# Kernel optimization log

Hardware: AMD Instinct MI355X
Metric: run time of the kernel (lower is better)

The kernel has to match this reference:

```python
import jax, jax.numpy as jnp
import numpy as np

EPS = 1e-10
NCE_T = 0.1
JSD_T = 1.0

def setup_inputs() -> dict:
    key = jax.random.key(0)
    k1, k2, k3, k4, k5 = jax.random.split(key, 5)
    N, D, C = 8192, 128, 1000
    return {
        'fs': jax.random.normal(k1, (N, D), dtype=jnp.float32),
        'ft': jax.random.normal(k2, (N, D), dtype=jnp.float32),
        'logit_s': jax.random.normal(k3, (N, C), dtype=jnp.float32),
        'logit_t': jax.random.normal(k4, (N, C), dtype=jnp.float32),
        'target': jax.random.randint(k5, (N,), 0, 100, dtype=jnp.int64),
    }

def _l2_normalize(x, axis=1, eps=1e-12):
    n = jnp.sqrt(jnp.sum(x * x, axis=axis, keepdims=True))
    return x / jnp.maximum(n, eps)

def _nce_loss(f1, f2, targets):
    f1 = _l2_normalize(f1)
    f2 = _l2_normalize(f2)
    # pos_mask[i,j] = 1 where targets[i] == targets[j] (same class, incl. diagonal)
    pos_mask = (targets[:, None] == targets[None, :]).astype(jnp.float32)  # [N,N]
    neg_mask = 1.0 - pos_mask
    # dist = ||f1_i - f2_j||^2 = 2 - 2 <f1_i, f2_j> for unit vectors -> cos = 1 - 0.5*dist = f1 @ f2.T
    cos = jnp.matmul(f1, f2.T)  # [N,N]
    ps = jax.nn.softmax(cos / NCE_T, axis=1)
    log_pos = -jnp.log(ps + EPS) * pos_mask
    log_neg = -jnp.log(1.0 - ps + EPS) * neg_mask
    row = log_pos.sum(1) / pos_mask.sum(1) + log_neg.sum(1) / neg_mask.sum(1)
    return row.mean()

def _jsd_loss(y_s, y_t):
    N = y_s.shape[0]
    log_ps = jax.nn.log_softmax(y_s / JSD_T, axis=1)
    log_pt = jax.nn.log_softmax(y_t / JSD_T, axis=1)
    pt = jnp.exp(log_pt)
    ps = jnp.exp(log_ps)
    # F.kl_div(input=log_p, target=q, reduction='sum') = sum(q * (log q - log_p))
    kl_st = jnp.sum(pt * (log_pt - log_ps)) * (JSD_T ** 2) / N
    kl_ts = jnp.sum(ps * (log_ps - log_pt)) * (JSD_T ** 2) / N
    return 0.5 * (kl_st + kl_ts)

def reference(fs, ft, logit_s, logit_t, target):
    return _nce_loss(fs, ft, target) + _jsd_loss(logit_s, logit_t)
```

## Files before the change

kernel.cpp:

```cpp
#include <hip/hip_runtime.h>
#include <hip/hip_bf16.h>

#define NN 8192
#define DD 128
#define CC 1000
#define LN2 0.69314718f
#define G_SCALE 14.42695041f
#define NSTRIP 16
#define JPER   512
#define NTILE  8
#define LROW   128
#define GRID_NCE 1024
#define JSD_BLOCKS 2048
#define PREP_GRID (JSD_BLOCKS + 1024 + 8)

typedef short v8s __attribute__((ext_vector_type(8)));
typedef float v4f __attribute__((ext_vector_type(4)));
typedef unsigned short u16;
typedef unsigned int u32;

typedef __attribute__((address_space(1))) const unsigned char ga_t;
typedef __attribute__((address_space(3))) unsigned char la_t;
#define GLOAD_LDS16(g, l) __builtin_amdgcn_global_load_lds((ga_t*)(g), (la_t*)(l), 16, 0, 0)

#if __has_builtin(__builtin_amdgcn_exp2f)
#define EXP2(x) __builtin_amdgcn_exp2f(x)
#else
#define EXP2(x) exp2f(x)
#endif
#if __has_builtin(__builtin_amdgcn_logf)
#define LOG2(x) __builtin_amdgcn_logf(x)
#else
#define LOG2(x) log2f(x)
#endif

static __device__ __forceinline__ float bf2f(u16 u) {
    union { float f; u32 i; } x; x.i = ((u32)u) << 16; return x.f;
}
static __device__ __forceinline__ u16 f2bf(float f) {
    u32 x = __float_as_uint(f);
    return (u16)((x + 0x7FFFu + ((x >> 16) & 1u)) >> 16);
}
static __device__ __forceinline__ float wsum(float v) {
    #pragma unroll
    for (int m = 1; m < 64; m <<= 1) v += __shfl_xor(v, m, 64);
    return v;
}
static __device__ __forceinline__ float wmax(float v) {
    #pragma unroll
    for (int m = 1; m < 64; m <<= 1) v = fmaxf(v, __shfl_xor(v, m, 64));
    return v;
}

__global__ __launch_bounds__(256) void prep_kernel(const void* __restrict__ fs,
                                                   const void* __restrict__ ft,
                                                   const int* __restrict__ traw,
                                                   const void* __restrict__ ls,
                                                   const void* __restrict__ lt,
                                                   u16* __restrict__ f1, u16* __restrict__ f2,
                                                   int* __restrict__ tgt32,
                                                   int* __restrict__ ghist,
                                                   float* __restrict__ sums) {
    __shared__ float sred[4];
    __shared__ int h[128];
    int b = blockIdx.x, tid = threadIdx.x;
    int w = tid >> 6, lane = tid & 63;

    if (b < JSD_BLOCKS) {
        int row = b * 4 + w;
        u32 wb = ((const u32*)ls)[(size_t)row * 500 + lane];
        unsigned e = (wb >> 7) & 0xFF;
        int isF32 = (__popcll(__ballot(e >= 100 && e <= 140)) < 32);

        float xs[16], xt[16];
        #pragma unroll
        for (int c = 0; c < 4; c++) {
            int idx = c * 256 + lane * 4;
            if (idx < CC) {
                if (isF32) {
                    float4 a = *(const float4*)((const float*)ls + (size_t)row * CC + idx);
                    float4 bb = *(const float4*)((const float*)lt + (size_t)row * CC + idx);
                    xs[c*4+0] = a.x; xs[c*4+1] = a.y; xs[c*4+2] = a.z; xs[c*4+3] = a.w;
                    xt[c*4+0] = bb.x; xt[c*4+1] = bb.y; xt[c*4+2] = bb.z; xt[c*4+3] = bb.w;
                } else {
                    ushort4 a = *(const ushort4*)((const u16*)ls + (size_t)row * CC + idx);
                    ushort4 bb = *(const ushort4*)((const u16*)lt + (size_t)row * CC + idx);
                    xs[c*4+0] = bf2f(a.x); xs[c*4+1] = bf2f(a.y); xs[c*4+2] = bf2f(a.z); xs[c*4+3] = bf2f(a.w);
                    xt[c*4+0] = bf2f(bb.x); xt[c*4+1] = bf2f(bb.y); xt[c*4+2] = bf2f(bb.z); xt[c*4+3] = bf2f(bb.w);
                }
            } else {
                #pragma unroll
                for (int q = 0; q < 4; q++) { xs[c*4+q] = -1e30f; xt[c*4+q] = -1e30f; }
            }
        }
        float ms = -1e30f, mt = -1e30f;
        #pragma unroll
        for (int q = 0; q < 16; q++) { ms = fmaxf(ms, xs[q]); mt = fmaxf(mt, xt[q]); }
        ms = wmax(ms); mt = wmax(mt);
        float es = 0.f, et = 0.f;
        #pragma unroll
        for (int q = 0; q < 16; q++) { es += __expf(xs[q] - ms); et += __expf(xt[q] - mt); }
        es = wsum(es); et = wsum(et);
        float lse_s = ms + __logf(es), lse_t = mt + __logf(et);
        float contrib = 0.f;
        #pragma unroll
        for (int q = 0; q < 16; q++) {
            float lps = xs[q] - lse_s, lpt = xt[q] - lse_t;
            contrib += (lpt - lps) * (__expf(lpt) - __expf(lps));
        }
        contrib = wsum(contrib);
        if (lane == 0) sred[w] = contrib;
        __syncthreads();
        if (tid == 0) atomicAdd(&sums[1], sred[0] + sred[1] + sred[2] + sred[3]);
    } else if (b < JSD_BLOCKS + 1024) {
        int nb = b - JSD_BLOCKS;
        #pragma unroll
        for (int r = 0; r < 4; r++) {
            int row4 = nb * 16 + w * 4 + r;
            const void* src; u16* dst; float gain; int row;
            if (row4 < NN) { src = fs; dst = f1; gain = G_SCALE; row = row4; }
            else           { src = ft; dst = f2; gain = 1.0f;    row = row4 - NN; }
            u32 wb = ((const u32*)src)[(size_t)row * 64 + lane];
            unsigned e = (wb >> 7) & 0xFF;
            int isF32 = (__popcll(__ballot(e >= 100 && e <= 140)) < 32);
            float x0, x1;
            if (isF32) {
                float2 v = ((const float2*)src)[(size_t)row * 64 + lane];
                x0 = v.x; x1 = v.y;
            } else {
                x0 = bf2f((u16)(wb & 0xFFFF));
                x1 = bf2f((u16)(wb >> 16));
            }
            float ss = wsum(x0 * x0 + x1 * x1);
            float sc = gain / fmaxf(sqrtf(ss), 1e-12f);
            u32 outw = (u32)f2bf(x0 * sc) | ((u32)f2bf(x1 * sc) << 16);
            ((u32*)dst)[(size_t)row * 64 + lane] = outw;
        }
    } else {
        int db = b - JSD_BLOCKS - 1024;
        if (tid < 128) h[tid] = 0;
        __syncthreads();
        #pragma unroll
        for (int r = 0; r < 4; r++) {
            int idx = db * 1024 + r * 256 + tid;
            int k = (idx >> 1) & 4095;
            int odd = traw[2 * k + 1];
            int is32 = (__ballot(odd != 0) != 0ull);
            int t = (is32 ? traw[idx] : traw[2 * idx]) & 127;
            tgt32[idx] = t;
            atomicAdd(&h[t], 1);
        }
        __syncthreads();
        if (tid < 128 && h[tid]) atomicAdd(&ghist[tid], h[tid]);
    }
}

__global__ __launch_bounds__(256) void main_kernel(const u16* __restrict__ f1,
                                                   const u16* __restrict__ f2,
                                                   const int* __restrict__ tgt,
                                                   float* __restrict__ Pp,
                                                   float* __restrict__ Qp,
                                                   float* __restrict__ Sp) {
    __shared__ u16 lds[2][64 * LROW];
    int bx = blockIdx.x;
    int tid = threadIdx.x;
    int w = tid >> 6, lane = tid & 63;

    int strip = bx & (NSTRIP - 1);
    int ib = bx >> 4;
    int quad = lane >> 4, lcol = lane & 15;
    int ibase = ib * 128 + w * 32;

    v8s a0[4], a1[4];
    #pragma unroll
    for (int t = 0; t < 4; t++) {
        int k = t * 32 + quad * 8;
        a0[t] = *(const v8s*)(f1 + (size_t)(ibase + lcol) * DD + k);
        a1[t] = *(const v8s*)(f1 + (size_t)(ibase + 16 + lcol) * DD + k);
    }
    int ti[8];
    #pragma unroll
    for (int a = 0; a < 2; a++)
        #pragma unroll
        for (int v = 0; v < 4; v++)
            ti[a * 4 + v] = tgt[ibase + a * 16 + quad * 4 + v];

    float P[8] = {}, Q[8] = {}, S[8] = {};

    int rrl = 4 * w + (lane >> 4);
    int cg = (lane & 15) ^ rrl;
    const u16* gb = f2 + (size_t)strip * JPER * DD + (size_t)rrl * DD + cg * 8;
    int ldsbase = 4 * w * 256;

    #pragma unroll
    for (int r = 0; r < 4; r++)
        GLOAD_LDS16(gb + (size_t)r * 16 * DD,
                    (unsigned char*)lds[0] + ldsbase + r * 16 * 256);

    for (int it = 0; it < NTILE; ++it) {
        __syncthreads();
        if (it + 1 < NTILE) {
            const u16* g2 = gb + (size_t)(it + 1) * 64 * DD;
            unsigned char* l2 = (unsigned char*)lds[(it + 1) & 1] + ldsbase;
            #pragma unroll
            for (int r = 0; r < 4; r++)
                GLOAD_LDS16(g2 + (size_t)r * 16 * DD, l2 + r * 16 * 256);
        }
        int jb = strip * JPER + it * 64;
        int tj0 = tgt[jb + lcol];
        int tj1 = tgt[jb + 16 + lcol];
        int tj2 = tgt[jb + 32 + lcol];
        int tj3 = tgt[jb + 48 + lcol];

        const u16* buf = lds[it & 1];
        v4f zero = {0.f, 0.f, 0.f, 0.f};
        v4f acc[8] = {zero, zero, zero, zero, zero, zero, zero, zero};
        #pragma unroll
        for (int t = 0; t < 4; t++) {
            int s = ((quad + 4 * t) ^ lcol) * 8;
            v8s b0 = *(const v8s*)(buf + (lcol)*LROW + s);
            v8s b1 = *(const v8s*)(buf + (16 + lcol) * LROW + s);
            v8s b2 = *(const v8s*)(buf + (32 + lcol) * LROW + s);
            v8s b3 = *(const v8s*)(buf + (48 + lcol) * LROW + s);
            acc[0] = __builtin_amdgcn_mfma_f32_16x16x32_bf16(a0[t], b0, acc[0], 0, 0, 0);
            acc[1] = __builtin_amdgcn_mfma_f32_16x16x32_bf16(a0[t], b1, acc[1], 0, 0, 0);
            acc[2] = __builtin_amdgcn_mfma_f32_16x16x32_bf16(a0[t], b2, acc[2], 0, 0, 0);
            acc[3] = __builtin_amdgcn_mfma_f32_16x16x32_bf16(a0[t], b3, acc[3], 0, 0, 0);
            acc[4] = __builtin_amdgcn_mfma_f32_16x16x32_bf16(a1[t], b0, acc[4], 0, 0, 0);
            acc[5] = __builtin_amdgcn_mfma_f32_16x16x32_bf16(a1[t], b1, acc[5], 0, 0, 0);
            acc[6] = __builtin_amdgcn_mfma_f32_16x16x32_bf16(a1[t], b2, acc[6], 0, 0, 0);
            acc[7] = __builtin_amdgcn_mfma_f32_16x16x32_bf16(a1[t], b3, acc[7], 0, 0, 0);
        }
        #pragma unroll
        for (int a = 0; a < 2; a++) {
            #pragma unroll
            for (int v = 0; v < 4; v++) {
                int t_i = ti[a * 4 + v];
                #pragma unroll
                for (int jf = 0; jf < 4; jf++) {
                    float s2 = acc[a * 4 + jf][v];
                    float e1 = EXP2(s2);
                    int tj = (jf == 0) ? tj0 : (jf == 1) ? tj1 : (jf == 2) ? tj2 : tj3;
                    bool pos = (tj == t_i);
                    P[a * 4 + v] += e1;
                    Q[a * 4 + v] += pos ? e1 : 0.0f;
                    S[a * 4 + v] += pos ? s2 : 0.0f;
                }
            }
        }
    }

    #pragma unroll
    for (int a = 0; a < 2; a++) {
        #pragma unroll
        for (int v = 0; v < 4; v++) {
            float p = P[a * 4 + v], q = Q[a * 4 + v], s = S[a * 4 + v];
            #pragma unroll
            for (int m = 1; m < 16; m <<= 1) {
                p += __shfl_xor(p, m, 64);
                q += __shfl_xor(q, m, 64);
                s += __shfl_xor(s, m, 64);
            }
            if (lcol == 0) {
                size_t idx = (size_t)strip * NN + ibase + a * 16 + quad * 4 + v;
                Pp[idx] = p;
                Qp[idx] = q;
                Sp[idx] = s;
            }
        }
    }
}

__global__ __launch_bounds__(256) void rowred_kernel(const float* __restrict__ Pp,
                                                     const float* __restrict__ Qp,
                                                     const float* __restrict__ Sp,
                                                     const int* __restrict__ tgt,
                                                     const int* __restrict__ ghist,
                                                     float* __restrict__ sums,
                                                     u32* __restrict__ out) {
    __shared__ float sb[4];
    __shared__ int lastf;
    int tid = threadIdx.x;

    int i = blockIdx.x * 256 + tid;
    float P = 0.f, Q = 0.f, S = 0.f;
    #pragma unroll
    for (int s = 0; s < NSTRIP; s++) {
        P += Pp[(size_t)s * NN + i];
        Q += Qp[(size_t)s * NN + i];
        S += Sp[(size_t)s * NN + i];
    }
    int cnt = ghist[tgt[i]];
    float pos = LN2 * LOG2(P) - LN2 * S / (float)cnt;
    float neg = (1.0f - Q / P) / (float)(NN - cnt);
    float l = wsum(pos + neg);
    if ((tid & 63) == 0) sb[tid >> 6] = l;
    __syncthreads();
    if (tid == 0) {
        atomicAdd(&sums[0], sb[0] + sb[1] + sb[2] + sb[3]);
        __threadfence();
        int* done = (int*)sums + 2;
        lastf = (atomicAdd(done, 1) == 31);
    }
    __syncthreads();
    if (!lastf) return;
    if (tid == 0) {
        float Lsum = __hip_atomic_load(&sums[0], __ATOMIC_RELAXED, __HIP_MEMORY_SCOPE_AGENT);
        float Jsum = __hip_atomic_load(&sums[1], __ATOMIC_RELAXED, __HIP_MEMORY_SCOPE_AGENT);
        float loss = (Lsum + 0.5f * Jsum) / (float)NN;
        u32 fb = __float_as_uint(loss);
        out[0] = (fb & 0xFFFF0000u) | (u32)f2bf(loss);
    }
}

extern "C" void kernel_launch(void* const* d_in, const int* in_sizes, int n_in,
                              void* d_out, int out_size, void* d_ws, size_t ws_size,
                              hipStream_t stream) {
    const void* fs = d_in[0];
    const void* ft = d_in[1];
    const void* ls = d_in[2];
    const void* lt = d_in[3];
    const int* tgt_raw = (const int*)d_in[4];

    char* wsp = (char*)d_ws;
    u16*   f1    = (u16*)(wsp + 0);
    u16*   f2    = (u16*)(wsp + 2097152);
    float* Pp    = (float*)(wsp + 4194304);
    float* Qp    = (float*)(wsp + 4718592);
    float* Sp    = (float*)(wsp + 5242880);
    float* sums  = (float*)(wsp + 5767168);
    int*   ghist = (int*)(wsp + 5767296);
    int*   tgt32 = (int*)(wsp + 5768192);

    hipMemsetAsync(wsp + 5767168, 0, 640, stream);
    prep_kernel<<<PREP_GRID, 256, 0, stream>>>(fs, ft, tgt_raw, ls, lt,
                                               f1, f2, tgt32, ghist, sums);
    main_kernel<<<GRID_NCE, 256, 0, stream>>>(f1, f2, tgt32, Pp, Qp, Sp);
    rowred_kernel<<<32, 256, 0, stream>>>(Pp, Qp, Sp, tgt32, ghist, sums, (u32*)d_out);
}
```

Measured before the change: 165.9 us.

## Move JSD work into the final reduction kernel and drop the memset

```diff
diff --git a/kernel.cpp b/kernel.cpp
--- a/kernel.cpp
+++ b/kernel.cpp
@@ -12,7 +12,9 @@
 #define LROW   128
 #define GRID_NCE 1024
 #define JSD_BLOCKS 2048
-#define PREP_GRID (JSD_BLOCKS + 1024 + 8)
+#define RED_BLOCKS 32
+#define GRID_JR (JSD_BLOCKS + RED_BLOCKS)
+#define DONE_TARGET GRID_JR
 
 typedef short v8s __attribute__((ext_vector_type(8)));
 typedef float v4f __attribute__((ext_vector_type(4)));
@@ -51,23 +53,198 @@
     for (int m = 1; m < 64; m <<= 1) v = fmaxf(v, __shfl_xor(v, m, 64));
     return v;
 }
+static __device__ __forceinline__ void finalize(float* sums, u32* out) {
+    float Lsum = __hip_atomic_load(&sums[0], __ATOMIC_RELAXED, __HIP_MEMORY_SCOPE_AGENT);
+    float Jsum = __hip_atomic_load(&sums[1], __ATOMIC_RELAXED, __HIP_MEMORY_SCOPE_AGENT);
+    float loss = (Lsum + 0.5f * Jsum) / (float)NN;
+    u32 fb = __float_as_uint(loss);
+    out[0] = (fb & 0xFFFF0000u) | (u32)f2bf(loss);
+}
 
 __global__ __launch_bounds__(256) void prep_kernel(const void* __restrict__ fs,
                                                    const void* __restrict__ ft,
                                                    const int* __restrict__ traw,
-                                                   const void* __restrict__ ls,
-                                                   const void* __restrict__ lt,
                                                    u16* __restrict__ f1, u16* __restrict__ f2,
                                                    int* __restrict__ tgt32,
                                                    int* __restrict__ ghist,
                                                    float* __restrict__ sums) {
-    __shared__ float sred[4];
     __shared__ int h[128];
     int b = blockIdx.x, tid = threadIdx.x;
     int w = tid >> 6, lane = tid & 63;
 
-    if (b < JSD_BLOCKS) {
-        int row = b * 4 + w;
+    if (b < 1024) {
+        #pragma unroll
+        for (int r = 0; r < 4; r++) {
+            int row4 = b * 16 + w * 4 + r;
+            const void* src; u16* dst; float gain; int row;
+            if (row4 < NN) { src = fs; dst = f1; gain = G_SCALE; row = row4; }
+            else           { src = ft; dst = f2; gain = 1.0f;    row = row4 - NN; }
+            u32 wb = ((const u32*)src)[(size_t)row * 64 + lane];
+            unsigned e = (wb >> 7) & 0xFF;
+            int isF32 = (__popcll(__ballot(e >= 100 && e <= 140)) < 32);
+            float x0, x1;
+            if (isF32) {
+                float2 v = ((const float2*)src)[(size_t)row * 64 + lane];
+                x0 = v.x; x1 = v.y;
+            } else {
+                x0 = bf2f((u16)(wb & 0xFFFF));
+                x1 = bf2f((u16)(wb >> 16));
+            }
+            float ss = wsum(x0 * x0 + x1 * x1);
+            float sc = gain / fmaxf(sqrtf(ss), 1e-12f);
+            u32 outw = (u32)f2bf(x0 * sc) | ((u32)f2bf(x1 * sc) << 16);
+            ((u32*)dst)[(size_t)row * 64 + lane] = outw;
+        }
+    } else {
+        if (tid < 4) sums[tid] = 0.0f;
+        if (tid < 128) h[tid] = 0;
+        __syncthreads();
+        for (int r = 0; r < 32; r++) {
+            int idx = r * 256 + tid;
+            int k = (idx >> 1) & 4095;
+            int odd = traw[2 * k + 1];
+            int is32 = (__ballot(odd != 0) != 0ull);
+            int t = (is32 ? traw[idx] : traw[2 * idx]) & 127;
+            tgt32[idx] = t;
+            atomicAdd(&h[t], 1);
+        }
+        __syncthreads();
+        if (tid < 128) ghist[tid] = h[tid];
+    }
+}
+
+__global__ __launch_bounds__(256) void main_kernel(const u16* __restrict__ f1,
+                                                   const u16* __restrict__ f2,
+                                                   const int* __restrict__ tgt,
+                                                   float* __restrict__ Pp,
+                                                   float* __restrict__ Qp,
+                                                   float* __restrict__ Sp) {
+    __shared__ u16 lds[2][64 * LROW];
+    int bx = blockIdx.x;
+    int tid = threadIdx.x;
+    int w = tid >> 6, lane = tid & 63;
+
+    int strip = bx & (NSTRIP - 1);
+    int ib = bx >> 4;
+    int quad = lane >> 4, lcol = lane & 15;
+    int ibase = ib * 128 + w * 32;
+
+    v8s a0[4], a1[4];
+    #pragma unroll
+    for (int t = 0; t < 4; t++) {
+        int k = t * 32 + quad * 8;
+        a0[t] = *(const v8s*)(f1 + (size_t)(ibase + lcol) * DD + k);
+        a1[t] = *(const v8s*)(f1 + (size_t)(ibase + 16 + lcol) * DD + k);
+    }
+    int ti[8];
+    #pragma unroll
+    for (int a = 0; a < 2; a++)
+        #pragma unroll
+        for (int v = 0; v < 4; v++)
+            ti[a * 4 + v] = tgt[ibase + a * 16 + quad * 4 + v];
+
+    float P[8] = {}, Q[8] = {}, S[8] = {};
+
+    int rrl = 4 * w + (lane >> 4);
+    int cg = (lane & 15) ^ rrl;
+    const u16* gb = f2 + (size_t)strip * JPER * DD + (size_t)rrl * DD + cg * 8;
+    int ldsbase = 4 * w * 256;
+
+    #pragma unroll
+    for (int r = 0; r < 4; r++)
+        GLOAD_LDS16(gb + (size_t)r * 16 * DD,
+                    (unsigned char*)lds[0] + ldsbase + r * 16 * 256);
+
+    for (int it = 0; it < NTILE; ++it) {
+        __syncthreads();
+        if (it + 1 < NTILE) {
+            const u16* g2 = gb + (size_t)(it + 1) * 64 * DD;
+            unsigned char* l2 = (unsigned char*)lds[(it + 1) & 1] + ldsbase;
+            #pragma unroll
+            for (int r = 0; r < 4; r++)
+                GLOAD_LDS16(g2 + (size_t)r * 16 * DD, l2 + r * 16 * 256);
+        }
+        int jb = strip * JPER + it * 64;
+        int tj0 = tgt[jb + lcol];
+        int tj1 = tgt[jb + 16 + lcol];
+        int tj2 = tgt[jb + 32 + lcol];
+        int tj3 = tgt[jb + 48 + lcol];
+
+        const u16* buf = lds[it & 1];
+        v4f zero = {0.f, 0.f, 0.f, 0.f};
+        v4f acc[8] = {zero, zero, zero, zero, zero, zero, zero, zero};
+        #pragma unroll
+        for (int t = 0; t < 4; t++) {
+            int s = ((quad + 4 * t) ^ lcol) * 8;
+            v8s b0 = *(const v8s*)(buf + (lcol)*LROW + s);
+            v8s b1 = *(const v8s*)(buf + (16 + lcol) * LROW + s);
+            v8s b2 = *(const v8s*)(buf + (32 + lcol) * LROW + s);
+            v8s b3 = *(const v8s*)(buf + (48 + lcol) * LROW + s);
+            acc[0] = __builtin_amdgcn_mfma_f32_16x16x32_bf16(a0[t], b0, acc[0], 0, 0, 0);
+            acc[1] = __builtin_amdgcn_mfma_f32_16x16x32_bf16(a0[t], b1, acc[1], 0, 0, 0);
+            acc[2] = __builtin_amdgcn_mfma_f32_16x16x32_bf16(a0[t], b2, acc[2], 0, 0, 0);
+            acc[3] = __builtin_amdgcn_mfma_f32_16x16x32_bf16(a0[t], b3, acc[3], 0, 0, 0);
+            acc[4] = __builtin_amdgcn_mfma_f32_16x16x32_bf16(a1[t], b0, acc[4], 0, 0, 0);
+            acc[5] = __builtin_amdgcn_mfma_f32_16x16x32_bf16(a1[t], b1, acc[5], 0, 0, 0);
+            acc[6] = __builtin_amdgcn_mfma_f32_16x16x32_bf16(a1[t], b2, acc[6], 0, 0, 0);
+            acc[7] = __builtin_amdgcn_mfma_f32_16x16x32_bf16(a1[t], b3, acc[7], 0, 0, 0);
+        }
+        #pragma unroll
+        for (int a = 0; a < 2; a++) {
+            #pragma unroll
+            for (int v = 0; v < 4; v++) {
+                int t_i = ti[a * 4 + v];
+                #pragma unroll
+                for (int jf = 0; jf < 4; jf++) {
+                    float s2 = acc[a * 4 + jf][v];
+                    float e1 = EXP2(s2);
+                    int tj = (jf == 0) ? tj0 : (jf == 1) ? tj1 : (jf == 2) ? tj2 : tj3;
+                    bool pos = (tj == t_i);
+                    P[a * 4 + v] += e1;
+                    Q[a * 4 + v] += pos ? e1 : 0.0f;
+                    S[a * 4 + v] += pos ? s2 : 0.0f;
+                }
+            }
+        }
+    }
+
+    #pragma unroll
+    for (int a = 0; a < 2; a++) {
+        #pragma unroll
+        for (int v = 0; v < 4; v++) {
+            float p = P[a * 4 + v], q = Q[a * 4 + v], s = S[a * 4 + v];
+            #pragma unroll
+            for (int m = 1; m < 16; m <<= 1) {
+                p += __shfl_xor(p, m, 64);
+                q += __shfl_xor(q, m, 64);
+                s += __shfl_xor(s, m, 64);
+            }
+            if (lcol == 0) {
+                size_t idx = (size_t)strip * NN + ibase + a * 16 + quad * 4 + v;
+                Pp[idx] = p;
+                Qp[idx] = q;
+                Sp[idx] = s;
+            }
+        }
+    }
+}
+
+__global__ __launch_bounds__(256) void jsdred_kernel(const void* __restrict__ ls,
+                                                     const void* __restrict__ lt,
+                                                     const float* __restrict__ Pp,
+                                                     const float* __restrict__ Qp,
+                                                     const float* __restrict__ Sp,
+                                                     const int* __restrict__ tgt,
+                                                     const int* __restrict__ ghist,
+                                                     float* __restrict__ sums,
+                                                     u32* __restrict__ out) {
+    __shared__ float sred[4];
+    int bx = blockIdx.x;
+    int tid = threadIdx.x;
+    int w = tid >> 6, lane = tid & 63;
+
+    if (bx < JSD_BLOCKS) {
+        int row = bx * 4 + w;
         u32 wb = ((const u32*)ls)[(size_t)row * 500 + lane];
         unsigned e = (wb >> 7) & 0xFF;
         int isF32 = (__popcll(__ballot(e >= 100 && e <= 140)) < 32);
@@ -111,205 +288,31 @@
         contrib = wsum(contrib);
         if (lane == 0) sred[w] = contrib;
         __syncthreads();
-        if (tid == 0) atomicAdd(&sums[1], sred[0] + sred[1] + sred[2] + sred[3]);
-    } else if (b < JSD_BLOCKS + 1024) {
-        int nb = b - JSD_BLOCKS;
-        #pragma unroll
-        for (int r = 0; r < 4; r++) {
-            int row4 = nb * 16 + w * 4 + r;
-            const void* src; u16* dst; float gain; int row;
-            if (row4 < NN) { src = fs; dst = f1; gain = G_SCALE; row = row4; }
-            else           { src = ft; dst = f2; gain = 1.0f;    row = row4 - NN; }
-            u32 wb = ((const u32*)src)[(size_t)row * 64 + lane];
-            unsigned e = (wb >> 7) & 0xFF;
-            int isF32 = (__popcll(__ballot(e >= 100 && e <= 140)) < 32);
-            float x0, x1;
-            if (isF32) {
-                float2 v = ((const float2*)src)[(size_t)row * 64 + lane];
-                x0 = v.x; x1 = v.y;
-            } else {
-                x0 = bf2f((u16)(wb & 0xFFFF));
-                x1 = bf2f((u16)(wb >> 16));
-            }
-            float ss = wsum(x0 * x0 + x1 * x1);
-            float sc = gain / fmaxf(sqrtf(ss), 1e-12f);
-            u32 outw = (u32)f2bf(x0 * sc) | ((u32)f2bf(x1 * sc) << 16);
-            ((u32*)dst)[(size_t)row * 64 + lane] = outw;
+        if (tid == 0) {
+            atomicAdd(&sums[1], sred[0] + sred[1] + sred[2] + sred[3]);
+            __threadfence();
+            if (atomicAdd((int*)sums + 2, 1) == DONE_TARGET - 1) finalize(sums, out);
         }
     } else {
-        int db = b - JSD_BLOCKS - 1024;
-        if (tid < 128) h[tid] = 0;
-        __syncthreads();
-        #pragma unroll
-        for (int r = 0; r < 4; r++) {
-            int idx = db * 1024 + r * 256 + tid;
-            int k = (idx >> 1) & 4095;
-            int odd = traw[2 * k + 1];
-            int is32 = (__ballot(odd != 0) != 0ull);
-            int t = (is32 ? traw[idx] : traw[2 * idx]) & 127;
-            tgt32[idx] = t;
-            atomicAdd(&h[t], 1);
-        }
-        __syncthreads();
-        if (tid < 128 && h[tid]) atomicAdd(&ghist[tid], h[tid]);
-    }
-}
-
-__global__ __launch_bounds__(256) void main_kernel(const u16* __restrict__ f1,
-                                                   const u16* __restrict__ f2,
-                                                   const int* __restrict__ tgt,
-                                                   float* __restrict__ Pp,
-                                                   float* __restrict__ Qp,
-                                                   float* __restrict__ Sp) {
-    __shared__ u16 lds[2][64 * LROW];
-    int bx = blockIdx.x;
-    int tid = threadIdx.x;
-    int w = tid >> 6, lane = tid & 63;
-
-    int strip = bx & (NSTRIP - 1);
-    int ib = bx >> 4;
-    int quad = lane >> 4, lcol = lane & 15;
-    int ibase = ib * 128 + w * 32;
-
-    v8s a0[4], a1[4];
-    #pragma unroll
-    for (int t = 0; t < 4; t++) {
-        int k = t * 32 + quad * 8;
-        a0[t] = *(const v8s*)(f1 + (size_t)(ibase + lcol) * DD + k);
-        a1[t] = *(const v8s*)(f1 + (size_t)(ibase + 16 + lcol) * DD + k);
-    }
-    int ti[8];
-    #pragma unroll
-    for (int a = 0; a < 2; a++)
-        #pragma unroll
-        for (int v = 0; v < 4; v++)
-            ti[a * 4 + v] = tgt[ibase + a * 16 + quad * 4 + v];
-
-    float P[8] = {}, Q[8] = {}, S[8] = {};
-
-    int rrl = 4 * w + (lane >> 4);
-    int cg = (lane & 15) ^ rrl;
-    const u16* gb = f2 + (size_t)strip * JPER * DD + (size_t)rrl * DD + cg * 8;
-    int ldsbase = 4 * w * 256;
-
-    #pragma unroll
-    for (int r = 0; r < 4; r++)
-        GLOAD_LDS16(gb + (size_t)r * 16 * DD,
-                    (unsigned char*)lds[0] + ldsbase + r * 16 * 256);
-
-    for (int it = 0; it < NTILE; ++it) {
-        __syncthreads();
-        if (it + 1 < NTILE) {
-            const u16* g2 = gb + (size_t)(it + 1) * 64 * DD;
-            unsigned char* l2 = (unsigned char*)lds[(it + 1) & 1] + ldsbase;
-            #pragma unroll
-            for (int r = 0; r < 4; r++)
-                GLOAD_LDS16(g2 + (size_t)r * 16 * DD, l2 + r * 16 * 256);
-        }
-        int jb = strip * JPER + it * 64;
-        int tj0 = tgt[jb + lcol];
-        int tj1 = tgt[jb + 16 + lcol];
-        int tj2 = tgt[jb + 32 + lcol];
-        int tj3 = tgt[jb + 48 + lcol];
-
-        const u16* buf = lds[it & 1];
-        v4f zero = {0.f, 0.f, 0.f, 0.f};
-        v4f acc[8] = {zero, zero, zero, zero, zero, zero, zero, zero};
-        #pragma unroll
-        for (int t = 0; t < 4; t++) {
-            int s = ((quad + 4 * t) ^ lcol) * 8;
-            v8s b0 = *(const v8s*)(buf + (lcol)*LROW + s);
-            v8s b1 = *(const v8s*)(buf + (16 + lcol) * LROW + s);
-            v8s b2 = *(const v8s*)(buf + (32 + lcol) * LROW + s);
-            v8s b3 = *(const v8s*)(buf + (48 + lcol) * LROW + s);
-            acc[0] = __builtin_amdgcn_mfma_f32_16x16x32_bf16(a0[t], b0, acc[0], 0, 0, 0);
-            acc[1] = __builtin_amdgcn_mfma_f32_16x16x32_bf16(a0[t], b1, acc[1], 0, 0, 0);
-            acc[2] = __builtin_amdgcn_mfma_f32_16x16x32_bf16(a0[t], b2, acc[2], 0, 0, 0);
-            acc[3] = __builtin_amdgcn_mfma_f32_16x16x32_bf16(a0[t], b3, acc[3], 0, 0, 0);
-            acc[4] = __builtin_amdgcn_mfma_f32_16x16x32_bf16(a1[t], b0, acc[4], 0, 0, 0);
-            acc[5] = __builtin_amdgcn_mfma_f32_16x16x32_bf16(a1[t], b1, acc[5], 0, 0, 0);
-            acc[6] = __builtin_amdgcn_mfma_f32_16x16x32_bf16(a1[t], b2, acc[6], 0, 0, 0);
-            acc[7] = __builtin_amdgcn_mfma_f32_16x16x32_bf16(a1[t], b3, acc[7], 0, 0, 0);
-        }
-        #pragma unroll
-        for (int a = 0; a < 2; a++) {
-            #pragma unroll
-            for (int v = 0; v < 4; v++) {
-                int t_i = ti[a * 4 + v];
-                #pragma unroll
-                for (int jf = 0; jf < 4; jf++) {
-                    float s2 = acc[a * 4 + jf][v];
-                    float e1 = EXP2(s2);
-                    int tj = (jf == 0) ? tj0 : (jf == 1) ? tj1 : (jf == 2) ? tj2 : tj3;
-                    bool pos = (tj == t_i);
-                    P[a * 4 + v] += e1;
-                    Q[a * 4 + v] += pos ? e1 : 0.0f;
-                    S[a * 4 + v] += pos ? s2 : 0.0f;
-                }
-            }
-        }
-    }
-
-    #pragma unroll
-    for (int a = 0; a < 2; a++) {
-        #pragma unroll
-        for (int v = 0; v < 4; v++) {
-            float p = P[a * 4 + v], q = Q[a * 4 + v], s = S[a * 4 + v];
-            #pragma unroll
-            for (int m = 1; m < 16; m <<= 1) {
-                p += __shfl_xor(p, m, 64);
-                q += __shfl_xor(q, m, 64);
-                s += __shfl_xor(s, m, 64);
-            }
-            if (lcol == 0) {
-                size_t idx = (size_t)strip * NN + ibase + a * 16 + quad * 4 + v;
-                Pp[idx] = p;
-                Qp[idx] = q;
-                Sp[idx] = s;
-            }
-        }
-    }
-}
-
-__global__ __launch_bounds__(256) void rowred_kernel(const float* __restrict__ Pp,
-                                                     const float* __restrict__ Qp,
-                                                     const float* __restrict__ Sp,
-                                                     const int* __restrict__ tgt,
-                                                     const int* __restrict__ ghist,
-                                                     float* __restrict__ sums,
-                                                     u32* __restrict__ out) {
-    __shared__ float sb[4];
-    __shared__ int lastf;
-    int tid = threadIdx.x;
-
-    int i = blockIdx.x * 256 + tid;
-    float P = 0.f, Q = 0.f, S = 0.f;
-    #pragma unroll
-    for (int s = 0; s < NSTRIP; s++) {
-        P += Pp[(size_t)s * NN + i];
-        Q += Qp[(size_t)s * NN + i];
-        S += Sp[(size_t)s * NN + i];
-    }
-    int cnt = ghist[tgt[i]];
-    float pos = LN2 * LOG2(P) - LN2 * S / (float)cnt;
-    float neg = (1.0f - Q / P) / (float)(NN - cnt);
-    float l = wsum(pos + neg);
-    if ((tid & 63) == 0) sb[tid >> 6] = l;
-    __syncthreads();
-    if (tid == 0) {
-        atomicAdd(&sums[0], sb[0] + sb[1] + sb[2] + sb[3]);
-        __threadfence();
-        int* done = (int*)sums + 2;
-        lastf = (atomicAdd(done, 1) == 31);
-    }
-    __syncthreads();
-    if (!lastf) return;
-    if (tid == 0) {
-        float Lsum = __hip_atomic_load(&sums[0], __ATOMIC_RELAXED, __HIP_MEMORY_SCOPE_AGENT);
-        float Jsum = __hip_atomic_load(&sums[1], __ATOMIC_RELAXED, __HIP_MEMORY_SCOPE_AGENT);
-        float loss = (Lsum + 0.5f * Jsum) / (float)NN;
-        u32 fb = __float_as_uint(loss);
-        out[0] = (fb & 0xFFFF0000u) | (u32)f2bf(loss);
+        int i = (bx - JSD_BLOCKS) * 256 + tid;
+        float P = 0.f, Q = 0.f, S = 0.f;
+        #pragma unroll
+        for (int s = 0; s < NSTRIP; s++) {
+            P += Pp[(size_t)s * NN + i];
+            Q += Qp[(size_t)s * NN + i];
+            S += Sp[(size_t)s * NN + i];
+        }
+        int cnt = ghist[tgt[i]];
+        float pos = LN2 * LOG2(P) - LN2 * S / (float)cnt;
+        float neg = (1.0f - Q / P) / (float)(NN - cnt);
+        float l = wsum(pos + neg);
+        if ((tid & 63) == 0) sred[tid >> 6] = l;
+        __syncthreads();
+        if (tid == 0) {
+            atomicAdd(&sums[0], sred[0] + sred[1] + sred[2] + sred[3]);
+            __threadfence();
+            if (atomicAdd((int*)sums + 2, 1) == DONE_TARGET - 1) finalize(sums, out);
+        }
     }
 }
 
@@ -332,9 +335,8 @@
     int*   ghist = (int*)(wsp + 5767296);
     int*   tgt32 = (int*)(wsp + 5768192);
 
-    hipMemsetAsync(wsp + 5767168, 0, 640, stream);
-    prep_kernel<<<PREP_GRID, 256, 0, stream>>>(fs, ft, tgt_raw, ls, lt,
-                                               f1, f2, tgt32, ghist, sums);
+    prep_kernel<<<1025, 256, 0, stream>>>(fs, ft, tgt_raw, f1, f2, tgt32, ghist, sums);
     main_kernel<<<GRID_NCE, 256, 0, stream>>>(f1, f2, tgt32, Pp, Qp, Sp);
-    rowred_kernel<<<32, 256, 0, stream>>>(Pp, Qp, Sp, tgt32, ghist, sums, (u32*)d_out);
-}
+    jsdred_kernel<<<GRID_JR, 256, 0, stream>>>(ls, lt, Pp, Qp, Sp, tgt32, ghist, sums,
+                                               (u32*)d_out);
+}
```

After: 226.3 us. 1.36x slower.

## Interleave JSD logit blocks with NCE matmul blocks in one kernel

Applied to the files above, without the earlier changes.

```diff
diff --git a/kernel.cpp b/kernel.cpp
--- a/kernel.cpp
+++ b/kernel.cpp
@@ -10,9 +10,8 @@
 #define JPER   512
 #define NTILE  8
 #define LROW   128
-#define GRID_NCE 1024
-#define JSD_BLOCKS 2048
-#define PREP_GRID (JSD_BLOCKS + 1024 + 8)
+#define GRID_MAIN 3072
+#define RED_BLOCKS 32
 
 typedef short v8s __attribute__((ext_vector_type(8)));
 typedef float v4f __attribute__((ext_vector_type(4)));
@@ -55,19 +54,179 @@
 __global__ __launch_bounds__(256) void prep_kernel(const void* __restrict__ fs,
                                                    const void* __restrict__ ft,
                                                    const int* __restrict__ traw,
-                                                   const void* __restrict__ ls,
-                                                   const void* __restrict__ lt,
                                                    u16* __restrict__ f1, u16* __restrict__ f2,
                                                    int* __restrict__ tgt32,
                                                    int* __restrict__ ghist,
                                                    float* __restrict__ sums) {
-    __shared__ float sred[4];
     __shared__ int h[128];
     int b = blockIdx.x, tid = threadIdx.x;
     int w = tid >> 6, lane = tid & 63;
 
-    if (b < JSD_BLOCKS) {
-        int row = b * 4 + w;
+    if (b < 1024) {
+        #pragma unroll
+        for (int r = 0; r < 4; r++) {
+            int row4 = b * 16 + w * 4 + r;
+            const void* src; u16* dst; float gain; int row;
+            if (row4 < NN) { src = fs; dst = f1; gain = G_SCALE; row = row4; }
+            else           { src = ft; dst = f2; gain = 1.0f;    row = row4 - NN; }
+            u32 wb = ((const u32*)src)[(size_t)row * 64 + lane];
+            unsigned e = (wb >> 7) & 0xFF;
+            int isF32 = (__popcll(__ballot(e >= 100 && e <= 140)) < 32);
+            float x0, x1;
+            if (isF32) {
+                float2 v = ((const float2*)src)[(size_t)row * 64 + lane];
+                x0 = v.x; x1 = v.y;
+            } else {
+                x0 = bf2f((u16)(wb & 0xFFFF));
+                x1 = bf2f((u16)(wb >> 16));
+            }
+            float ss = wsum(x0 * x0 + x1 * x1);
+            float sc = gain / fmaxf(sqrtf(ss), 1e-12f);
+            u32 outw = (u32)f2bf(x0 * sc) | ((u32)f2bf(x1 * sc) << 16);
+            ((u32*)dst)[(size_t)row * 64 + lane] = outw;
+        }
+    } else {
+        if (tid < 4) sums[tid] = 0.0f;
+        if (tid < 128) h[tid] = 0;
+        __syncthreads();
+        for (int r = 0; r < 32; r++) {
+            int idx = r * 256 + tid;
+            int k = (idx >> 1) & 4095;
+            int odd = traw[2 * k + 1];
+            int is32 = (__ballot(odd != 0) != 0ull);
+            int t = (is32 ? traw[idx] : traw[2 * idx]) & 127;
+            tgt32[idx] = t;
+            atomicAdd(&h[t], 1);
+        }
+        __syncthreads();
+        if (tid < 128) ghist[tid] = h[tid];
+    }
+}
+
+__global__ __launch_bounds__(256) void main_kernel(const u16* __restrict__ f1,
+                                                   const u16* __restrict__ f2,
+                                                   const int* __restrict__ tgt,
+                                                   const void* __restrict__ ls,
+                                                   const void* __restrict__ lt,
+                                                   float* __restrict__ Pp,
+                                                   float* __restrict__ Qp,
+                                                   float* __restrict__ Sp,
+                                                   float* __restrict__ sums) {
+    __shared__ u16 lds[2][64 * LROW];
+    __shared__ float sred[4];
+    int bx = blockIdx.x;
+    int tid = threadIdx.x;
+    int w = tid >> 6, lane = tid & 63;
+    int sel = bx % 3;
+
+    if (sel == 0) {
+        int id = bx / 3;
+        int strip = id & (NSTRIP - 1);
+        int ib = id >> 4;
+        int quad = lane >> 4, lcol = lane & 15;
+        int ibase = ib * 128 + w * 32;
+
+        v8s a0[4], a1[4];
+        #pragma unroll
+        for (int t = 0; t < 4; t++) {
+            int k = t * 32 + quad * 8;
+            a0[t] = *(const v8s*)(f1 + (size_t)(ibase + lcol) * DD + k);
+            a1[t] = *(const v8s*)(f1 + (size_t)(ibase + 16 + lcol) * DD + k);
+        }
+        int ti[8];
+        #pragma unroll
+        for (int a = 0; a < 2; a++)
+            #pragma unroll
+            for (int v = 0; v < 4; v++)
+                ti[a * 4 + v] = tgt[ibase + a * 16 + quad * 4 + v];
+
+        float P[8] = {}, Q[8] = {}, S[8] = {};
+
+        int rrl = 4 * w + (lane >> 4);
+        int cg = (lane & 15) ^ rrl;
+        const u16* gb = f2 + (size_t)strip * JPER * DD + (size_t)rrl * DD + cg * 8;
+        int ldsbase = 4 * w * 256;
+
+        #pragma unroll
+        for (int r = 0; r < 4; r++)
+            GLOAD_LDS16(gb + (size_t)r * 16 * DD,
+                        (unsigned char*)lds[0] + ldsbase + r * 16 * 256);
+
+        for (int it = 0; it < NTILE; ++it) {
+            __syncthreads();
+            if (it + 1 < NTILE) {
+                const u16* g2 = gb + (size_t)(it + 1) * 64 * DD;
+                unsigned char* l2 = (unsigned char*)lds[(it + 1) & 1] + ldsbase;
+                #pragma unroll
+                for (int r = 0; r < 4; r++)
+                    GLOAD_LDS16(g2 + (size_t)r * 16 * DD, l2 + r * 16 * 256);
+            }
+            int jb = strip * JPER + it * 64;
+            int tj0 = tgt[jb + lcol];
+            int tj1 = tgt[jb + 16 + lcol];
+            int tj2 = tgt[jb + 32 + lcol];
+            int tj3 = tgt[jb + 48 + lcol];
+
+            const u16* buf = lds[it & 1];
+            v4f zero = {0.f, 0.f, 0.f, 0.f};
+            v4f acc[8] = {zero, zero, zero, zero, zero, zero, zero, zero};
+            #pragma unroll
+            for (int t = 0; t < 4; t++) {
+                int s = ((quad + 4 * t) ^ lcol) * 8;
+                v8s b0 = *(const v8s*)(buf + (lcol)*LROW + s);
+                v8s b1 = *(const v8s*)(buf + (16 + lcol) * LROW + s);
+                v8s b2 = *(const v8s*)(buf + (32 + lcol) * LROW + s);
+                v8s b3 = *(const v8s*)(buf + (48 + lcol) * LROW + s);
+                acc[0] = __builtin_amdgcn_mfma_f32_16x16x32_bf16(a0[t], b0, acc[0], 0, 0, 0);
+                acc[1] = __builtin_amdgcn_mfma_f32_16x16x32_bf16(a0[t], b1, acc[1], 0, 0, 0);
+                acc[2] = __builtin_amdgcn_mfma_f32_16x16x32_bf16(a0[t], b2, acc[2], 0, 0, 0);
+                acc[3] = __builtin_amdgcn_mfma_f32_16x16x32_bf16(a0[t], b3, acc[3], 0, 0, 0);
+                acc[4] = __builtin_amdgcn_mfma_f32_16x16x32_bf16(a1[t], b0, acc[4], 0, 0, 0);
+                acc[5] = __builtin_amdgcn_mfma_f32_16x16x32_bf16(a1[t], b1, acc[5], 0, 0, 0);
+                acc[6] = __builtin_amdgcn_mfma_f32_16x16x32_bf16(a1[t], b2, acc[6], 0, 0, 0);
+                acc[7] = __builtin_amdgcn_mfma_f32_16x16x32_bf16(a1[t], b3, acc[7], 0, 0, 0);
+            }
+            #pragma unroll
+            for (int a = 0; a < 2; a++) {
+                #pragma unroll
+                for (int v = 0; v < 4; v++) {
+                    int t_i = ti[a * 4 + v];
+                    #pragma unroll
+                    for (int jf = 0; jf < 4; jf++) {
+                        float s2 = acc[a * 4 + jf][v];
+                        float e1 = EXP2(s2);
+                        int tj = (jf == 0) ? tj0 : (jf == 1) ? tj1 : (jf == 2) ? tj2 : tj3;
+                        bool pos = (tj == t_i);
+                        P[a * 4 + v] += e1;
+                        Q[a * 4 + v] += pos ? e1 : 0.0f;
+                        S[a * 4 + v] += pos ? s2 : 0.0f;
+                    }
+                }
+            }
+        }
+
+        #pragma unroll
+        for (int a = 0; a < 2; a++) {
+            #pragma unroll
+            for (int v = 0; v < 4; v++) {
+                float p = P[a * 4 + v], q = Q[a * 4 + v], s = S[a * 4 + v];
+                #pragma unroll
+                for (int m = 1; m < 16; m <<= 1) {
+                    p += __shfl_xor(p, m, 64);
+                    q += __shfl_xor(q, m, 64);
+                    s += __shfl_xor(s, m, 64);
+                }
+                if (lcol == 0) {
+                    size_t idx = (size_t)strip * NN + ibase + a * 16 + quad * 4 + v;
+                    Pp[idx] = p;
+                    Qp[idx] = q;
+                    Sp[idx] = s;
+                }
+            }
+        }
+    } else {
+        int id = (bx / 3) * 2 + sel - 1;
+        int row = id * 4 + w;
         u32 wb = ((const u32*)ls)[(size_t)row * 500 + lane];
         unsigned e = (wb >> 7) & 0xFF;
         int isF32 = (__popcll(__ballot(e >= 100 && e <= 140)) < 32);
@@ -93,6 +252,11 @@
                 for (int q = 0; q < 4; q++) { xs[c*4+q] = -1e30f; xt[c*4+q] = -1e30f; }
             }
         }
+        #pragma unroll
+        for (int q = 0; q < 16; q++) {
+            asm volatile("" : "+v"(xs[q]));
+            asm volatile("" : "+v"(xt[q]));
+        }
         float ms = -1e30f, mt = -1e30f;
         #pragma unroll
         for (int q = 0; q < 16; q++) { ms = fmaxf(ms, xs[q]); mt = fmaxf(mt, xt[q]); }
@@ -112,162 +276,6 @@
         if (lane == 0) sred[w] = contrib;
         __syncthreads();
         if (tid == 0) atomicAdd(&sums[1], sred[0] + sred[1] + sred[2] + sred[3]);
-    } else if (b < JSD_BLOCKS + 1024) {
-        int nb = b - JSD_BLOCKS;
-        #pragma unroll
-        for (int r = 0; r < 4; r++) {
-            int row4 = nb * 16 + w * 4 + r;
-            const void* src; u16* dst; float gain; int row;
-            if (row4 < NN) { src = fs; dst = f1; gain = G_SCALE; row = row4; }
-            else           { src = ft; dst = f2; gain = 1.0f;    row = row4 - NN; }
-            u32 wb = ((const u32*)src)[(size_t)row * 64 + lane];
-            unsigned e = (wb >> 7) & 0xFF;
-            int isF32 = (__popcll(__ballot(e >= 100 && e <= 140)) < 32);
-            float x0, x1;
-            if (isF32) {
-                float2 v = ((const float2*)src)[(size_t)row * 64 + lane];
-                x0 = v.x; x1 = v.y;
-            } else {
-                x0 = bf2f((u16)(wb & 0xFFFF));
-                x1 = bf2f((u16)(wb >> 16));
-            }
-            float ss = wsum(x0 * x0 + x1 * x1);
-            float sc = gain / fmaxf(sqrtf(ss), 1e-12f);
-            u32 outw = (u32)f2bf(x0 * sc) | ((u32)f2bf(x1 * sc) << 16);
-            ((u32*)dst)[(size_t)row * 64 + lane] = outw;
-        }
-    } else {
-        int db = b - JSD_BLOCKS - 1024;
-        if (tid < 128) h[tid] = 0;
-        __syncthreads();
-        #pragma unroll
-        for (int r = 0; r < 4; r++) {
-            int idx = db * 1024 + r * 256 + tid;
-            int k = (idx >> 1) & 4095;
-            int odd = traw[2 * k + 1];
-            int is32 = (__ballot(odd != 0) != 0ull);
-            int t = (is32 ? traw[idx] : traw[2 * idx]) & 127;
-            tgt32[idx] = t;
-            atomicAdd(&h[t], 1);
-        }
-        __syncthreads();
-        if (tid < 128 && h[tid]) atomicAdd(&ghist[tid], h[tid]);
-    }
-}
-
-__global__ __launch_bounds__(256) void main_kernel(const u16* __restrict__ f1,
-                                                   const u16* __restrict__ f2,
-                                                   const int* __restrict__ tgt,
-                                                   float* __restrict__ Pp,
-                                                   float* __restrict__ Qp,
-                                                   float* __restrict__ Sp) {
-    __shared__ u16 lds[2][64 * LROW];
-    int bx = blockIdx.x;
-    int tid = threadIdx.x;
-    int w = tid >> 6, lane = tid & 63;
-
-    int strip = bx & (NSTRIP - 1);
-    int ib = bx >> 4;
-    int quad = lane >> 4, lcol = lane & 15;
-    int ibase = ib * 128 + w * 32;
-
-    v8s a0[4], a1[4];
-    #pragma unroll
-    for (int t = 0; t < 4; t++) {
-        int k = t * 32 + quad * 8;
-        a0[t] = *(const v8s*)(f1 + (size_t)(ibase + lcol) * DD + k);
-        a1[t] = *(const v8s*)(f1 + (size_t)(ibase + 16 + lcol) * DD + k);
-    }
-    int ti[8];
-    #pragma unroll
-    for (int a = 0; a < 2; a++)
-        #pragma unroll
-        for (int v = 0; v < 4; v++)
-            ti[a * 4 + v] = tgt[ibase + a * 16 + quad * 4 + v];
-
-    float P[8] = {}, Q[8] = {}, S[8] = {};
-
-    int rrl = 4 * w + (lane >> 4);
-    int cg = (lane & 15) ^ rrl;
-    const u16* gb = f2 + (size_t)strip * JPER * DD + (size_t)rrl * DD + cg * 8;
-    int ldsbase = 4 * w * 256;
-
-    #pragma unroll
-    for (int r = 0; r < 4; r++)
-        GLOAD_LDS16(gb + (size_t)r * 16 * DD,
-                    (unsigned char*)lds[0] + ldsbase + r * 16 * 256);
-
-    for (int it = 0; it < NTILE; ++it) {
-        __syncthreads();
-        if (it + 1 < NTILE) {
-            const u16* g2 = gb + (size_t)(it + 1) * 64 * DD;
-            unsigned char* l2 = (unsigned char*)lds[(it + 1) & 1] + ldsbase;
-            #pragma unroll
-            for (int r = 0; r < 4; r++)
-                GLOAD_LDS16(g2 + (size_t)r * 16 * DD, l2 + r * 16 * 256);
-        }
-        int jb = strip * JPER + it * 64;
-        int tj0 = tgt[jb + lcol];
-        int tj1 = tgt[jb + 16 + lcol];
-        int tj2 = tgt[jb + 32 + lcol];
-        int tj3 = tgt[jb + 48 + lcol];
-
-        const u16* buf = lds[it & 1];
-        v4f zero = {0.f, 0.f, 0.f, 0.f};
-        v4f acc[8] = {zero, zero, zero, zero, zero, zero, zero, zero};
-        #pragma unroll
-        for (int t = 0; t < 4; t++) {
-            int s = ((quad + 4 * t) ^ lcol) * 8;
-            v8s b0 = *(const v8s*)(buf + (lcol)*LROW + s);
-            v8s b1 = *(const v8s*)(buf + (16 + lcol) * LROW + s);
-            v8s b2 = *(const v8s*)(buf + (32 + lcol) * LROW + s);
-            v8s b3 = *(const v8s*)(buf + (48 + lcol) * LROW + s);
-            acc[0] = __builtin_amdgcn_mfma_f32_16x16x32_bf16(a0[t], b0, acc[0], 0, 0, 0);
-            acc[1] = __builtin_amdgcn_mfma_f32_16x16x32_bf16(a0[t], b1, acc[1], 0, 0, 0);
-            acc[2] = __builtin_amdgcn_mfma_f32_16x16x32_bf16(a0[t], b2, acc[2], 0, 0, 0);
-            acc[3] = __builtin_amdgcn_mfma_f32_16x16x32_bf16(a0[t], b3, acc[3], 0, 0, 0);
-            acc[4] = __builtin_amdgcn_mfma_f32_16x16x32_bf16(a1[t], b0, acc[4], 0, 0, 0);
-            acc[5] = __builtin_amdgcn_mfma_f32_16x16x32_bf16(a1[t], b1, acc[5], 0, 0, 0);
-            acc[6] = __builtin_amdgcn_mfma_f32_16x16x32_bf16(a1[t], b2, acc[6], 0, 0, 0);
-            acc[7] = __builtin_amdgcn_mfma_f32_16x16x32_bf16(a1[t], b3, acc[7], 0, 0, 0);
-        }
-        #pragma unroll
-        for (int a = 0; a < 2; a++) {
-            #pragma unroll
-            for (int v = 0; v < 4; v++) {
-                int t_i = ti[a * 4 + v];
-                #pragma unroll
-                for (int jf = 0; jf < 4; jf++) {
-                    float s2 = acc[a * 4 + jf][v];
-                    float e1 = EXP2(s2);
-                    int tj = (jf == 0) ? tj0 : (jf == 1) ? tj1 : (jf == 2) ? tj2 : tj3;
-                    bool pos = (tj == t_i);
-                    P[a * 4 + v] += e1;
-                    Q[a * 4 + v] += pos ? e1 : 0.0f;
-                    S[a * 4 + v] += pos ? s2 : 0.0f;
-                }
-            }
-        }
-    }
-
-    #pragma unroll
-    for (int a = 0; a < 2; a++) {
-        #pragma unroll
-        for (int v = 0; v < 4; v++) {
-            float p = P[a * 4 + v], q = Q[a * 4 + v], s = S[a * 4 + v];
-            #pragma unroll
-            for (int m = 1; m < 16; m <<= 1) {
-                p += __shfl_xor(p, m, 64);
-                q += __shfl_xor(q, m, 64);
-                s += __shfl_xor(s, m, 64);
-            }
-            if (lcol == 0) {
-                size_t idx = (size_t)strip * NN + ibase + a * 16 + quad * 4 + v;
-                Pp[idx] = p;
-                Qp[idx] = q;
-                Sp[idx] = s;
-            }
-        }
     }
 }
 
@@ -300,7 +308,7 @@
         atomicAdd(&sums[0], sb[0] + sb[1] + sb[2] + sb[3]);
         __threadfence();
         int* done = (int*)sums + 2;
-        lastf = (atomicAdd(done, 1) == 31);
+        lastf = (atomicAdd(done, 1) == RED_BLOCKS - 1);
     }
     __syncthreads();
     if (!lastf) return;
@@ -332,9 +340,8 @@
     int*   ghist = (int*)(wsp + 5767296);
     int*   tgt32 = (int*)(wsp + 5768192);
 
-    hipMemsetAsync(wsp + 5767168, 0, 640, stream);
-    prep_kernel<<<PREP_GRID, 256, 0, stream>>>(fs, ft, tgt_raw, ls, lt,
-                                               f1, f2, tgt32, ghist, sums);
-    main_kernel<<<GRID_NCE, 256, 0, stream>>>(f1, f2, tgt32, Pp, Qp, Sp);
-    rowred_kernel<<<32, 256, 0, stream>>>(Pp, Qp, Sp, tgt32, ghist, sums, (u32*)d_out);
-}
+    prep_kernel<<<1025, 256, 0, stream>>>(fs, ft, tgt_raw, f1, f2, tgt32, ghist, sums);
+    main_kernel<<<GRID_MAIN, 256, 0, stream>>>(f1, f2, tgt32, ls, lt, Pp, Qp, Sp, sums);
+    rowred_kernel<<<RED_BLOCKS, 256, 0, stream>>>(Pp, Qp, Sp, tgt32, ghist, sums,
+                                                  (u32*)d_out);
+}
```

Measured after the change: 164.6 us. About the same (-0.7%).
